# Kernel optimization log

Hardware: AMD Instinct MI355X
Metric: run time of the kernel (lower is better)

## Reference

```python
import jax, jax.numpy as jnp
import numpy as np

NUM_HEADS = 8

def setup_inputs() -> dict:
    key = jax.random.key(0)
    ks = jax.random.split(key, 12)
    T, B, C, D = 2048, 4, 512, 512
    s = 1.0 / np.sqrt(C)
    return {
        "key_in": jax.random.normal(ks[0], (T, B, C), jnp.float32),
        "value_in": jax.random.normal(ks[1], (T, B, C), jnp.float32),
        "query_in": jax.random.normal(ks[2], (T, B, C), jnp.float32),
        "Wk": jax.random.normal(ks[3], (C, D), jnp.float32) * s,
        "bk": jax.random.normal(ks[4], (D,), jnp.float32) * 0.01,
        "Wv": jax.random.normal(ks[5], (C, D), jnp.float32) * s,
        "bv": jax.random.normal(ks[6], (D,), jnp.float32) * 0.01,
        "Wq": jax.random.normal(ks[7], (C, D), jnp.float32) * s,
        "bq": jax.random.normal(ks[8], (D,), jnp.float32) * 0.01,
        "Wo": jax.random.normal(ks[9], (D, D), jnp.float32) * (1.0 / np.sqrt(D)),
        "bo": jax.random.normal(ks[10], (D,), jnp.float32) * 0.01,
    }

def reference(key_in, value_in, query_in, Wk, bk, Wv, bv, Wq, bq, Wo, bo):
    T, B, C = query_in.shape
    D = Wq.shape[1]
    H = NUM_HEADS
    hd = D // H
    scale = 1.0 / np.sqrt(hd).astype(np.float32)
    # Linear projections on (T, B, C) -> (T, B, D), then the original's
    # row-major view(B, -1, H, hd) followed by transpose(1, 2) -> (B, H, T, hd)
    def proj(x, W, b):
        y = x @ W + b                      # (T, B, D)
        return y.reshape(B, -1, H, hd).transpose(0, 2, 1, 3)  # (B, H, T, hd)
    q = proj(query_in, Wq, bq)
    k = proj(key_in, Wk, bk)
    v = proj(value_in, Wv, bv)
    scores = jnp.einsum("bhqd,bhkd->bhqk", q, k) * scale  # (B, H, T, T)
    attn = jax.nn.softmax(scores, axis=-1)
    x = jnp.einsum("bhqk,bhkd->bhqd", attn, v)            # (B, H, T, hd)
    x = x.transpose(0, 2, 1, 3).reshape(T, B, D)          # matches .view(T, B, d_model)
    return x @ Wo + bo
```

## Files before the change

kernel.cpp:

```cpp
#include <hip/hip_runtime.h>
#include <math.h>

#define MROWS 8192
#define DM    512
#define SEQL  2048
#define HDIM  64
#define NSPLIT 2

typedef __attribute__((ext_vector_type(4))) float floatx4;
typedef _Float16 half2v __attribute__((ext_vector_type(2)));
typedef _Float16 half4v __attribute__((ext_vector_type(4)));
typedef _Float16 half8v __attribute__((ext_vector_type(8)));

#define CEXP 0.18033688011f

__device__ __forceinline__ void gll16(const void* g, void* l) {
    __builtin_amdgcn_global_load_lds(
        (const __attribute__((address_space(1))) unsigned int*)g,
        (__attribute__((address_space(3))) unsigned int*)l, 16, 0, 0);
}

__device__ __forceinline__ half4v pack4(float a, float b, float c, float d) {
    half2v lo = __builtin_bit_cast(half2v, __builtin_amdgcn_cvt_pkrtz(a, b));
    half2v hi = __builtin_bit_cast(half2v, __builtin_amdgcn_cvt_pkrtz(c, d));
    half4v r;
    r[0] = lo[0]; r[1] = lo[1]; r[2] = hi[0]; r[3] = hi[1];
    return r;
}

__global__ __launch_bounds__(256) void transw(const float* __restrict__ w0,
                                              const float* __restrict__ w1,
                                              const float* __restrict__ w2,
                                              const float* __restrict__ w3,
                                              _Float16* __restrict__ t0,
                                              _Float16* __restrict__ t1,
                                              _Float16* __restrict__ t2,
                                              _Float16* __restrict__ t3) {
    __shared__ float tile[32][33];
    const float* W = blockIdx.z == 0 ? w0 : (blockIdx.z == 1 ? w1 : (blockIdx.z == 2 ? w2 : w3));
    _Float16* T = blockIdx.z == 0 ? t0 : (blockIdx.z == 1 ? t1 : (blockIdx.z == 2 ? t2 : t3));
    const float sc = (blockIdx.z == 0) ? CEXP : 1.0f;
    const int tx = threadIdx.x & 31, ty = threadIdx.x >> 5;
    const int x = blockIdx.x * 32 + tx;
    const int y0 = blockIdx.y * 32;
#pragma unroll
    for (int i = 0; i < 4; ++i)
        tile[ty + i * 8][tx] = W[(size_t)(y0 + ty + i * 8) * DM + x];
    __syncthreads();
    const int xo = y0 + tx;
#pragma unroll
    for (int i = 0; i < 4; ++i)
        T[(size_t)(blockIdx.x * 32 + ty + i * 8) * DM + xo] = (_Float16)(tile[tx][ty + i * 8] * sc);
}

__global__ __launch_bounds__(256, 3) void proj_gemm(
        const float* __restrict__ q32, const float* __restrict__ k32, const float* __restrict__ v32,
        const _Float16* __restrict__ Wq, const _Float16* __restrict__ Wk, const _Float16* __restrict__ Wv,
        const float* __restrict__ bq, const float* __restrict__ bk, const float* __restrict__ bv,
        _Float16* __restrict__ Qo, _Float16* __restrict__ Ko, _Float16* __restrict__ Vto) {
    __shared__ _Float16 As[128 * 64];
    __shared__ _Float16 Bs[128 * 64];
    const int z = blockIdx.z;
    const float* A32    = z == 0 ? q32 : (z == 1 ? k32 : v32);
    const _Float16* Bt  = z == 0 ? Wq : (z == 1 ? Wk : Wv);
    const float* bias   = z == 0 ? bq : (z == 1 ? bk : bv);
    const float bscale  = z == 0 ? CEXP : 1.0f;

    const int tid = threadIdx.x;
    const int w = tid >> 6, wr = w >> 1, wc = w & 1;
    const int l15 = tid & 15, quad = (tid & 63) >> 4;
    const int m0 = blockIdx.x * 128, n0 = blockIdx.y * 128;

    const int arow = tid >> 1, ah = tid & 1;
    const float* Asrc = &A32[(size_t)(m0 + arow) * DM + ah * 32];
    _Float16* Adst = &As[arow * 64];
    const int asw = arow & 7;

    floatx4 acc[4][4];
#pragma unroll
    for (int i = 0; i < 4; ++i)
#pragma unroll
        for (int j = 0; j < 4; ++j) acc[i][j] = (floatx4){0.f, 0.f, 0.f, 0.f};

    for (int kt = 0; kt < DM / 64; ++kt) {
        __syncthreads();
        floatx4 f[8];
        {
            const float* s = Asrc + (size_t)kt * 64;
#pragma unroll
            for (int q = 0; q < 8; ++q) f[q] = *(const floatx4*)&s[q * 4];
        }
#pragma unroll
        for (int i = 0; i < 4; ++i) {
            const int c = i * 256 + tid;
            const int row = c >> 3, g = c & 7;
            const int kg = g ^ (row & 7);
            gll16(&Bt[(size_t)(n0 + row) * DM + kt * 64 + kg * 8], &Bs[c * 8]);
        }
#pragma unroll
        for (int t = 0; t < 4; ++t) {
            half8v o;
            o[0] = (_Float16)f[2 * t][0]; o[1] = (_Float16)f[2 * t][1];
            o[2] = (_Float16)f[2 * t][2]; o[3] = (_Float16)f[2 * t][3];
            o[4] = (_Float16)f[2 * t + 1][0]; o[5] = (_Float16)f[2 * t + 1][1];
            o[6] = (_Float16)f[2 * t + 1][2]; o[7] = (_Float16)f[2 * t + 1][3];
            const int g = ah * 4 + t;
            *(half8v*)&Adst[(g ^ asw) * 8] = o;
        }
        __syncthreads();
#pragma unroll
        for (int ks = 0; ks < 2; ++ks) {
            half8v af[4], bf[4];
#pragma unroll
            for (int i = 0; i < 4; ++i) {
                const int row = wr * 64 + i * 16 + l15;
                af[i] = *(const half8v*)&As[row * 64 + (((ks * 4 + quad)) ^ (row & 7)) * 8];
            }
#pragma unroll
            for (int j = 0; j < 4; ++j) {
                const int row = wc * 64 + j * 16 + l15;
                bf[j] = *(const half8v*)&Bs[row * 64 + (((ks * 4 + quad)) ^ (row & 7)) * 8];
            }
#pragma unroll
            for (int i = 0; i < 4; ++i)
#pragma unroll
                for (int j = 0; j < 4; ++j)
                    acc[i][j] = __builtin_amdgcn_mfma_f32_16x16x32_f16(af[i], bf[j], acc[i][j], 0, 0, 0);
        }
    }
#pragma unroll
    for (int j = 0; j < 4; ++j) {
        const int col = n0 + wc * 64 + j * 16 + l15;
        const float bv4 = bias[col] * bscale;
#pragma unroll
        for (int i = 0; i < 4; ++i) {
            const int rb = m0 + wr * 64 + i * 16 + quad * 4;
            if (z == 2) {
                const int g = rb >> 11, seq = rb & 2047;
                half4v pv;
#pragma unroll
                for (int r = 0; r < 4; ++r) pv[r] = (_Float16)(acc[i][j][r] + bv4);
                *(half4v*)&Vto[((size_t)g * DM + col) * SEQL + seq] = pv;
            } else {
                _Float16* oh = z == 0 ? Qo : Ko;
#pragma unroll
                for (int r = 0; r < 4; ++r)
                    oh[(size_t)(rb + r) * DM + col] = (_Float16)(acc[i][j][r] + bv4);
            }
        }
    }
}

__global__ __launch_bounds__(256, 4) void out_gemm(
        const _Float16* __restrict__ Op0, const _Float16* __restrict__ Op1,
        const float* __restrict__ lp,
        const _Float16* __restrict__ Wo, const float* __restrict__ bo,
        float* __restrict__ out) {
    __shared__ _Float16 Bs[256 * 64];
    __shared__ _Float16 As[32 * 64];
    const int tid = threadIdx.x;
    const int w = tid >> 6;
    const int l15 = tid & 15, quad = (tid & 63) >> 4;
    const int n0 = blockIdx.x * 256, m0 = blockIdx.y * 32;

    floatx4 acc[2][4];
#pragma unroll
    for (int i = 0; i < 2; ++i)
#pragma unroll
        for (int j = 0; j < 4; ++j) acc[i][j] = (floatx4){0.f, 0.f, 0.f, 0.f};

    for (int kt = 0; kt < DM / 64; ++kt) {
        __syncthreads();
#pragma unroll
        for (int i = 0; i < 8; ++i) {
            const int c = i * 256 + tid;
            const int row = c >> 3, g = c & 7;
            const int kg = g ^ (row & 7);
            gll16(&Wo[(size_t)(n0 + row) * DM + kt * 64 + kg * 8], &Bs[c * 8]);
        }
        {
            const int c = tid;
            const int row = c >> 3, g = c & 7;
            const int kg = g ^ (row & 7);
            const int grow = m0 + row;
            const size_t off = (size_t)grow * DM + kt * 64 + kg * 8;
            const half8v a = *(const half8v*)&Op0[off];
            const half8v b = *(const half8v*)&Op1[off];
            const float inv = 1.0f / (lp[(size_t)grow * 8 + kt] +
                                      lp[((size_t)MROWS + grow) * 8 + kt]);
            half8v s;
#pragma unroll
            for (int e = 0; e < 8; ++e)
                s[e] = (_Float16)(((float)a[e] + (float)b[e]) * inv);
            *(half8v*)&As[c * 8] = s;
        }
        __syncthreads();
#pragma unroll
        for (int ks = 0; ks < 2; ++ks) {
            half8v af[2], bfr[4];
#pragma unroll
            for (int i = 0; i < 2; ++i) {
                const int row = i * 16 + l15;
                af[i] = *(const half8v*)&As[row * 64 + ((ks * 4 + quad) ^ (row & 7)) * 8];
            }
#pragma unroll
            for (int j = 0; j < 4; ++j) {
                const int row = w * 64 + j * 16 + l15;
                bfr[j] = *(const half8v*)&Bs[row * 64 + ((ks * 4 + quad) ^ (row & 7)) * 8];
            }
#pragma unroll
            for (int i = 0; i < 2; ++i)
#pragma unroll
                for (int j = 0; j < 4; ++j)
                    acc[i][j] = __builtin_amdgcn_mfma_f32_16x16x32_f16(af[i], bfr[j], acc[i][j], 0, 0, 0);
        }
    }
#pragma unroll
    for (int j = 0; j < 4; ++j) {
        const int col = n0 + w * 64 + j * 16 + l15;
        const float bv4 = bo[col];
#pragma unroll
        for (int i = 0; i < 2; ++i) {
            const int rb = m0 + i * 16 + quad * 4;
#pragma unroll
            for (int r = 0; r < 4; ++r)
                out[(size_t)(rb + r) * DM + col] = acc[i][j][r] + bv4;
        }
    }
}

__global__ __launch_bounds__(256, 4) void attn_mfma(const _Float16* __restrict__ Q16,
                                                    const _Float16* __restrict__ K16,
                                                    const _Float16* __restrict__ Vt,
                                                    _Float16* __restrict__ Opart,
                                                    float* __restrict__ lpart) {
    __shared__ _Float16 Ks[2][64 * 64];
    __shared__ _Float16 Vs[2][64 * 64];

    const int tid  = threadIdx.x;
    const int lane = tid & 63;
    const int l15  = lane & 15;
    const int quad = lane >> 4;

    const int pair  = blockIdx.y;
    const int split = blockIdx.z;
    const int grp   = pair >> 3;
    const int h     = pair & 7;
    const int q0    = blockIdx.x * 128;
    const int rQ    = grp * SEQL + q0 + (tid >> 6) * 32;
    const int cb    = h * HDIM;
    const int NIT   = (SEQL / 64) / NSPLIT;
    const int kt0   = split * NIT;

    const _Float16* Kbase = K16 + (size_t)grp * SEQL * DM + cb;
    const _Float16* Vbase = Vt + (size_t)grp * DM * SEQL + (size_t)cb * SEQL;

    half8v qf[2][2];
#pragma unroll
    for (int qt = 0; qt < 2; ++qt)
#pragma unroll
        for (int ks = 0; ks < 2; ++ks)
            qf[qt][ks] = *(const half8v*)&Q16[(size_t)(rQ + qt * 16 + l15) * DM + cb + ks * 32 + quad * 8];

    floatx4 oacc[2][4], lacc[2];
#pragma unroll
    for (int qt = 0; qt < 2; ++qt) {
        lacc[qt] = (floatx4){0.f, 0.f, 0.f, 0.f};
#pragma unroll
        for (int dt = 0; dt < 4; ++dt) oacc[qt][dt] = (floatx4){0.f, 0.f, 0.f, 0.f};
    }
    half4v ones;
    ones[0] = (_Float16)1.f; ones[1] = (_Float16)1.f; ones[2] = (_Float16)1.f; ones[3] = (_Float16)1.f;

#define STAGE(KT, B)                                                            \
    {                                                                           \
        _Float16* ksb = &Ks[B][0];                                              \
        _Float16* vsb = &Vs[B][0];                                              \
        _Pragma("unroll")                                                       \
        for (int i_ = 0; i_ < 4; ++i_) {                                        \
            const int c_ = i_ * 256 + tid;                                      \
            if (c_ < 512) {                                                     \
                const int key_ = c_ >> 3, g_ = c_ & 7;                          \
                const int dg_ = g_ ^ (key_ & 7);                                \
                gll16(&Kbase[(size_t)((KT) * 64 + key_) * DM + dg_ * 8],        \
                      &ksb[c_ * 8]);                                            \
            } else {                                                            \
                const int cv_ = c_ - 512;                                      \
                const int d_ = cv_ >> 3, g_ = cv_ & 7;                          \
                const int kg_ = g_ ^ (d_ & 7);                                  \
                gll16(&Vbase[(size_t)d_ * SEQL + (KT) * 64 + kg_ * 8],          \
                      &vsb[cv_ * 8]);                                           \
            }                                                                   \
        }                                                                       \
    }

    STAGE(kt0, 0)

    for (int it = 0; it < NIT; ++it) {
        const int cur = it & 1;
        __syncthreads();
        if (it + 1 < NIT) STAGE(kt0 + it + 1, cur ^ 1)

        const _Float16* ksb = &Ks[cur][0];
        const _Float16* vsb = &Vs[cur][0];

        floatx4 st[4][2];
#pragma unroll
        for (int ktile = 0; ktile < 4; ++ktile) {
            const int key = ktile * 16 + l15;
            const half8v kf0 = *(const half8v*)&ksb[key * 64 + ((0 + quad) ^ (key & 7)) * 8];
            const half8v kf1 = *(const half8v*)&ksb[key * 64 + ((4 + quad) ^ (key & 7)) * 8];
#pragma unroll
            for (int qt = 0; qt < 2; ++qt) {
                floatx4 z = {0.f, 0.f, 0.f, 0.f};
                z = __builtin_amdgcn_mfma_f32_16x16x32_f16(kf0, qf[qt][0], z, 0, 0, 0);
                st[ktile][qt] = __builtin_amdgcn_mfma_f32_16x16x32_f16(kf1, qf[qt][1], z, 0, 0, 0);
            }
        }

        half4v pa[4][2];
#pragma unroll
        for (int ktile = 0; ktile < 4; ++ktile)
#pragma unroll
            for (int qt = 0; qt < 2; ++qt)
                pa[ktile][qt] = pack4(__builtin_amdgcn_exp2f(st[ktile][qt][0]),
                                      __builtin_amdgcn_exp2f(st[ktile][qt][1]),
                                      __builtin_amdgcn_exp2f(st[ktile][qt][2]),
                                      __builtin_amdgcn_exp2f(st[ktile][qt][3]));

#pragma unroll
        for (int qt = 0; qt < 2; ++qt)
#pragma unroll
            for (int ktile = 0; ktile < 4; ++ktile)
                lacc[qt] = __builtin_amdgcn_mfma_f32_16x16x16f16(pa[ktile][qt], ones, lacc[qt], 0, 0, 0);

#pragma unroll
        for (int dt = 0; dt < 4; ++dt) {
            const int d = dt * 16 + l15;
#pragma unroll
            for (int ktile = 0; ktile < 4; ++ktile) {
                const int G = ktile * 2 + (quad >> 1);
                const int slot = G ^ (d & 7);
                const half4v vf = *(const half4v*)&vsb[d * 64 + slot * 8 + (quad & 1) * 4];
#pragma unroll
                for (int qt = 0; qt < 2; ++qt)
                    oacc[qt][dt] = __builtin_amdgcn_mfma_f32_16x16x16f16(pa[ktile][qt], vf, oacc[qt][dt], 0, 0, 0);
            }
        }
    }

    _Float16* Op = Opart + (size_t)split * MROWS * DM;
#pragma unroll
    for (int qt = 0; qt < 2; ++qt)
#pragma unroll
        for (int r = 0; r < 4; ++r) {
            const int qrow = rQ + qt * 16 + quad * 4 + r;
            const size_t rowoff = (size_t)qrow * DM + cb;
#pragma unroll
            for (int dt = 0; dt < 4; ++dt)
                Op[rowoff + dt * 16 + l15] = (_Float16)oacc[qt][dt][r];
            if (l15 == 0)
                lpart[((size_t)split * MROWS + qrow) * 8 + h] = lacc[qt][r];
        }
}

extern "C" void kernel_launch(void* const* d_in, const int* in_sizes, int n_in,
                              void* d_out, int out_size, void* d_ws, size_t ws_size,
                              hipStream_t stream) {
    const float* key_in   = (const float*)d_in[0];
    const float* value_in = (const float*)d_in[1];
    const float* query_in = (const float*)d_in[2];
    const float* Wk = (const float*)d_in[3];
    const float* bk = (const float*)d_in[4];
    const float* Wv = (const float*)d_in[5];
    const float* bv = (const float*)d_in[6];
    const float* Wq = (const float*)d_in[7];
    const float* bq = (const float*)d_in[8];
    const float* Wo = (const float*)d_in[9];
    const float* bo = (const float*)d_in[10];
    float* out = (float*)d_out;

    const size_t MAT = (size_t)MROWS * DM;
    _Float16* Q16  = (_Float16*)d_ws;
    _Float16* K16  = Q16 + MAT;
    _Float16* Vtb  = K16 + MAT;
    _Float16* Wqt  = Vtb + MAT;
    _Float16* Wkt  = Wqt + DM * DM;
    _Float16* Wvt  = Wkt + DM * DM;
    _Float16* Wot  = Wvt + DM * DM;
    float*    lpart = (float*)(Wot + DM * DM);
    _Float16* Opart = (_Float16*)(lpart + 2 * MROWS * 8);

    const dim3 blk(256);

    transw<<<dim3(16, 16, 4), blk, 0, stream>>>(Wq, Wk, Wv, Wo, Wqt, Wkt, Wvt, Wot);

    proj_gemm<<<dim3(MROWS / 128, DM / 128, 3), blk, 0, stream>>>(
        query_in, key_in, value_in, Wqt, Wkt, Wvt, bq, bk, bv, Q16, K16, Vtb);

    attn_mfma<<<dim3(SEQL / 128, 32, NSPLIT), blk, 0, stream>>>(Q16, K16, Vtb, Opart, lpart);

    out_gemm<<<dim3(2, MROWS / 32), blk, 0, stream>>>(
        Opart, Opart + MAT, lpart, Wot, bo, out);
}
```

Before: 200.0 us.

## Triple-buffer K/V tiles and software-pipeline QK^T one tile ahead in attention

Moves the K/V shared-memory staging from double to triple buffering, so loads are issued two tiles ahead. The QK^T matrix multiplies for the next tile now run between the exp/pack of the current tile and its PV multiplies, which should overlap transcendental work with MFMA work. A priority raise (s_setprio) wraps the PV MFMA block. The cost is more LDS per block and a launch-bounds occupancy hint lowered from 4 to 3, which may reduce latency hiding across waves. There is now one barrier per iteration, at the end of the loop.

```diff
diff --git a/kernel.cpp b/kernel.cpp
--- a/kernel.cpp
+++ b/kernel.cpp
@@ -229,13 +229,13 @@
     }
 }
 
-__global__ __launch_bounds__(256, 4) void attn_mfma(const _Float16* __restrict__ Q16,
+__global__ __launch_bounds__(256, 3) void attn_mfma(const _Float16* __restrict__ Q16,
                                                     const _Float16* __restrict__ K16,
                                                     const _Float16* __restrict__ Vt,
                                                     _Float16* __restrict__ Opart,
                                                     float* __restrict__ lpart) {
-    __shared__ _Float16 Ks[2][64 * 64];
-    __shared__ _Float16 Vs[2][64 * 64];
+    __shared__ _Float16 Ks[3][64 * 64];
+    __shared__ _Float16 Vs[3][64 * 64];
 
     const int tid  = threadIdx.x;
     const int lane = tid & 63;
@@ -285,7 +285,7 @@
                 gll16(&Kbase[(size_t)((KT) * 64 + key_) * DM + dg_ * 8],        \
                       &ksb[c_ * 8]);                                            \
             } else {                                                            \
-                const int cv_ = c_ - 512;                                      \
+                const int cv_ = c_ - 512;                                       \
                 const int d_ = cv_ >> 3, g_ = cv_ & 7;                          \
                 const int kg_ = g_ ^ (d_ & 7);                                  \
                 gll16(&Vbase[(size_t)d_ * SEQL + (KT) * 64 + kg_ * 8],          \
@@ -294,29 +294,33 @@
         }                                                                       \
     }
 
+    floatx4 st[4][2];
+#define QKT(BUF)                                                                \
+    {                                                                           \
+        const _Float16* ksb = &Ks[BUF][0];                                      \
+        _Pragma("unroll")                                                       \
+        for (int ktile = 0; ktile < 4; ++ktile) {                               \
+            const int key = ktile * 16 + l15;                                   \
+            const half8v kf0 = *(const half8v*)&ksb[key * 64 + ((0 + quad) ^ (key & 7)) * 8]; \
+            const half8v kf1 = *(const half8v*)&ksb[key * 64 + ((4 + quad) ^ (key & 7)) * 8]; \
+            _Pragma("unroll")                                                   \
+            for (int qt = 0; qt < 2; ++qt) {                                    \
+                floatx4 zz = {0.f, 0.f, 0.f, 0.f};                              \
+                zz = __builtin_amdgcn_mfma_f32_16x16x32_f16(kf0, qf[qt][0], zz, 0, 0, 0); \
+                st[ktile][qt] = __builtin_amdgcn_mfma_f32_16x16x32_f16(kf1, qf[qt][1], zz, 0, 0, 0); \
+            }                                                                   \
+        }                                                                       \
+    }
+
     STAGE(kt0, 0)
+    __syncthreads();
+    STAGE(kt0 + 1, 1)
+    QKT(0)
+    __syncthreads();
 
     for (int it = 0; it < NIT; ++it) {
-        const int cur = it & 1;
-        __syncthreads();
-        if (it + 1 < NIT) STAGE(kt0 + it + 1, cur ^ 1)
-
-        const _Float16* ksb = &Ks[cur][0];
-        const _Float16* vsb = &Vs[cur][0];
-
-        floatx4 st[4][2];
-#pragma unroll
-        for (int ktile = 0; ktile < 4; ++ktile) {
-            const int key = ktile * 16 + l15;
-            const half8v kf0 = *(const half8v*)&ksb[key * 64 + ((0 + quad) ^ (key & 7)) * 8];
-            const half8v kf1 = *(const half8v*)&ksb[key * 64 + ((4 + quad) ^ (key & 7)) * 8];
-#pragma unroll
-            for (int qt = 0; qt < 2; ++qt) {
-                floatx4 z = {0.f, 0.f, 0.f, 0.f};
-                z = __builtin_amdgcn_mfma_f32_16x16x32_f16(kf0, qf[qt][0], z, 0, 0, 0);
-                st[ktile][qt] = __builtin_amdgcn_mfma_f32_16x16x32_f16(kf1, qf[qt][1], z, 0, 0, 0);
-            }
-        }
+        const int cur = it % 3, nxt = (it + 1) % 3, nn = (it + 2) % 3;
+        if (it + 2 < NIT) STAGE(kt0 + it + 2, nn)
 
         half4v pa[4][2];
 #pragma unroll
@@ -328,6 +332,10 @@
                                       __builtin_amdgcn_exp2f(st[ktile][qt][2]),
                                       __builtin_amdgcn_exp2f(st[ktile][qt][3]));
 
+        if (it + 1 < NIT) QKT(nxt)
+
+        const _Float16* vsb = &Vs[cur][0];
+        __builtin_amdgcn_s_setprio(1);
 #pragma unroll
         for (int qt = 0; qt < 2; ++qt)
 #pragma unroll
@@ -347,6 +355,8 @@
                     oacc[qt][dt] = __builtin_amdgcn_mfma_f32_16x16x16f16(pa[ktile][qt], vf, oacc[qt][dt], 0, 0, 0);
             }
         }
+        __builtin_amdgcn_s_setprio(0);
+        __syncthreads();
     }
 
     _Float16* Op = Opart + (size_t)split * MROWS * DM;
```

New measurement: 204.3 us. 1.02x slower.

## Drop split-K attention; normalize in attention epilogue and load O directly

Applied to the files above, without the earlier changes.

Removes the two-way key split in the attention kernel. Each block now walks the full sequence, divides by the row sum itself and writes one normalized fp16 output. The output GEMM then loads that tile straight into LDS with async global-to-LDS copies, with no merging of partials. This cuts the partial-buffer traffic and the merge arithmetic, but halves the attention grid (512 blocks) and doubles the per-block loop length, which may reduce occupancy across the CUs.

```diff
diff --git a/kernel.cpp b/kernel.cpp
--- a/kernel.cpp
+++ b/kernel.cpp
@@ -5,7 +5,6 @@
 #define DM    512
 #define SEQL  2048
 #define HDIM  64
-#define NSPLIT 2
 
 typedef __attribute__((ext_vector_type(4))) float floatx4;
 typedef _Float16 half2v __attribute__((ext_vector_type(2)));
@@ -152,8 +151,7 @@
 }
 
 __global__ __launch_bounds__(256, 4) void out_gemm(
-        const _Float16* __restrict__ Op0, const _Float16* __restrict__ Op1,
-        const float* __restrict__ lp,
+        const _Float16* __restrict__ O16,
         const _Float16* __restrict__ Wo, const float* __restrict__ bo,
         float* __restrict__ out) {
     __shared__ _Float16 Bs[256 * 64];
@@ -163,6 +161,9 @@
     const int l15 = tid & 15, quad = (tid & 63) >> 4;
     const int n0 = blockIdx.x * 256, m0 = blockIdx.y * 32;
 
+    const int arow = tid >> 3, ag = tid & 7;
+    const int akg = ag ^ (arow & 7);
+
     floatx4 acc[2][4];
 #pragma unroll
     for (int i = 0; i < 2; ++i)
@@ -178,22 +179,7 @@
             const int kg = g ^ (row & 7);
             gll16(&Wo[(size_t)(n0 + row) * DM + kt * 64 + kg * 8], &Bs[c * 8]);
         }
-        {
-            const int c = tid;
-            const int row = c >> 3, g = c & 7;
-            const int kg = g ^ (row & 7);
-            const int grow = m0 + row;
-            const size_t off = (size_t)grow * DM + kt * 64 + kg * 8;
-            const half8v a = *(const half8v*)&Op0[off];
-            const half8v b = *(const half8v*)&Op1[off];
-            const float inv = 1.0f / (lp[(size_t)grow * 8 + kt] +
-                                      lp[((size_t)MROWS + grow) * 8 + kt]);
-            half8v s;
-#pragma unroll
-            for (int e = 0; e < 8; ++e)
-                s[e] = (_Float16)(((float)a[e] + (float)b[e]) * inv);
-            *(half8v*)&As[c * 8] = s;
-        }
+        gll16(&O16[(size_t)(m0 + arow) * DM + kt * 64 + akg * 8], &As[tid * 8]);
         __syncthreads();
 #pragma unroll
         for (int ks = 0; ks < 2; ++ks) {
@@ -232,8 +218,7 @@
 __global__ __launch_bounds__(256, 4) void attn_mfma(const _Float16* __restrict__ Q16,
                                                     const _Float16* __restrict__ K16,
                                                     const _Float16* __restrict__ Vt,
-                                                    _Float16* __restrict__ Opart,
-                                                    float* __restrict__ lpart) {
+                                                    _Float16* __restrict__ O16) {
     __shared__ _Float16 Ks[2][64 * 64];
     __shared__ _Float16 Vs[2][64 * 64];
 
@@ -243,14 +228,12 @@
     const int quad = lane >> 4;
 
     const int pair  = blockIdx.y;
-    const int split = blockIdx.z;
     const int grp   = pair >> 3;
     const int h     = pair & 7;
     const int q0    = blockIdx.x * 128;
     const int rQ    = grp * SEQL + q0 + (tid >> 6) * 32;
     const int cb    = h * HDIM;
-    const int NIT   = (SEQL / 64) / NSPLIT;
-    const int kt0   = split * NIT;
+    const int NIT   = SEQL / 64;
 
     const _Float16* Kbase = K16 + (size_t)grp * SEQL * DM + cb;
     const _Float16* Vbase = Vt + (size_t)grp * DM * SEQL + (size_t)cb * SEQL;
@@ -285,7 +268,7 @@
                 gll16(&Kbase[(size_t)((KT) * 64 + key_) * DM + dg_ * 8],        \
                       &ksb[c_ * 8]);                                            \
             } else {                                                            \
-                const int cv_ = c_ - 512;                                      \
+                const int cv_ = c_ - 512;                                       \
                 const int d_ = cv_ >> 3, g_ = cv_ & 7;                          \
                 const int kg_ = g_ ^ (d_ & 7);                                  \
                 gll16(&Vbase[(size_t)d_ * SEQL + (KT) * 64 + kg_ * 8],          \
@@ -294,12 +277,12 @@
         }                                                                       \
     }
 
-    STAGE(kt0, 0)
+    STAGE(0, 0)
 
     for (int it = 0; it < NIT; ++it) {
         const int cur = it & 1;
         __syncthreads();
-        if (it + 1 < NIT) STAGE(kt0 + it + 1, cur ^ 1)
+        if (it + 1 < NIT) STAGE(it + 1, cur ^ 1)
 
         const _Float16* ksb = &Ks[cur][0];
         const _Float16* vsb = &Vs[cur][0];
@@ -349,18 +332,16 @@
         }
     }
 
-    _Float16* Op = Opart + (size_t)split * MROWS * DM;
 #pragma unroll
     for (int qt = 0; qt < 2; ++qt)
 #pragma unroll
         for (int r = 0; r < 4; ++r) {
             const int qrow = rQ + qt * 16 + quad * 4 + r;
             const size_t rowoff = (size_t)qrow * DM + cb;
+            const float inv = 1.0f / lacc[qt][r];
 #pragma unroll
             for (int dt = 0; dt < 4; ++dt)
-                Op[rowoff + dt * 16 + l15] = (_Float16)oacc[qt][dt][r];
-            if (l15 == 0)
-                lpart[((size_t)split * MROWS + qrow) * 8 + h] = lacc[qt][r];
+                O16[rowoff + dt * 16 + l15] = (_Float16)(oacc[qt][dt][r] * inv);
         }
 }
 
@@ -388,8 +369,7 @@
     _Float16* Wkt  = Wqt + DM * DM;
     _Float16* Wvt  = Wkt + DM * DM;
     _Float16* Wot  = Wvt + DM * DM;
-    float*    lpart = (float*)(Wot + DM * DM);
-    _Float16* Opart = (_Float16*)(lpart + 2 * MROWS * 8);
+    _Float16* O16  = Wot + DM * DM;
 
     const dim3 blk(256);
 
@@ -398,8 +378,7 @@
     proj_gemm<<<dim3(MROWS / 128, DM / 128, 3), blk, 0, stream>>>(
         query_in, key_in, value_in, Wqt, Wkt, Wvt, bq, bk, bv, Q16, K16, Vtb);
 
-    attn_mfma<<<dim3(SEQL / 128, 32, NSPLIT), blk, 0, stream>>>(Q16, K16, Vtb, Opart, lpart);
-
-    out_gemm<<<dim3(2, MROWS / 32), blk, 0, stream>>>(
-        Opart, Opart + MAT, lpart, Wot, bo, out);
-}
+    attn_mfma<<<dim3(SEQL / 128, 32), blk, 0, stream>>>(Q16, K16, Vtb, O16);
+
+    out_gemm<<<dim3(2, MROWS / 32), blk, 0, stream>>>(O16, Wot, bo, out);
+}
```

Measured after the change: 199.4 us. Within noise of the previous version (-0.3%).
